# Kernel optimization log

Hardware: AMD Instinct MI355X
Metric: run time of the kernel (lower is better)

Reference implementation:

```python
import jax, jax.numpy as jnp
import numpy as np

NUM_HEADS = 8
ATTN_DIM = 512
DIM_HEAD = ATTN_DIM // NUM_HEADS
SCALE = DIM_HEAD ** -0.5
GN_EPS = 1e-5


def setup_inputs() -> dict:
    key = jax.random.key(0)
    k1, k2, k3 = jax.random.split(key, 3)
    B, H, W, C_IN, C_OUT = 8, 32, 32, 256, 256
    x = jax.random.normal(k1, (B, H, W, C_IN), dtype=jnp.float32)
    w_qkv = jax.random.normal(k2, (C_IN, 3 * ATTN_DIM), dtype=jnp.float32) * (C_IN ** -0.5)
    w_out = jax.random.normal(k3, (ATTN_DIM, C_OUT), dtype=jnp.float32) * (ATTN_DIM ** -0.5)
    b_out = jnp.zeros((C_OUT,), dtype=jnp.float32)
    gamma = jnp.ones((C_OUT,), dtype=jnp.float32)
    beta = jnp.zeros((C_OUT,), dtype=jnp.float32)
    return {"x": x, "w_qkv": w_qkv, "w_out": w_out, "b_out": b_out, "gamma": gamma, "beta": beta}


def reference(x, w_qkv, w_out, b_out, gamma, beta):
    B, H, W, _ = x.shape
    N = H * W
    # 1x1 conv QKV projection (no bias)
    qkv = jnp.einsum('bhwc,cd->bhwd', x, w_qkv)
    q, k, v = jnp.split(qkv, 3, axis=-1)
    # NHWC -> (B, heads, dim_head, HW), matching tf transpose+reshape
    def to_heads(t):
        return t.transpose(0, 3, 1, 2).reshape(B, NUM_HEADS, DIM_HEAD, N)
    q = to_heads(q) * SCALE
    k = to_heads(k)
    v = to_heads(v)
    # sim = q^T k over dim_head: (B, heads, N_q, N_k)
    sim = jnp.einsum('bhcn,bhcm->bhnm', q, k)
    attn = jax.nn.softmax(sim, axis=-1)  # includes the max-subtraction of the original
    # out = attn @ v^T: (B, heads, N, dim_head)
    out = jnp.einsum('bhnm,bhcm->bhnc', attn, v)
    # faithful tf.reshape((B,-1,H,W)) then NCHW->NHWC transpose
    out = out.reshape(B, -1, H, W).transpose(0, 2, 3, 1)  # (B, H, W, attn_dim)
    # output 1x1 conv (with bias) + GroupNorm(groups=1): normalize over (H, W, C) per sample
    y = jnp.einsum('bhwc,cd->bhwd', out, w_out) + b_out
    mean = jnp.mean(y, axis=(1, 2, 3), keepdims=True)
    var = jnp.var(y, axis=(1, 2, 3), keepdims=True)
    y = (y - mean) * jax.lax.rsqrt(var + GN_EPS)
    return y * gamma + beta
```

## Files before the change

### kernel.cpp

```cpp
#include <hip/hip_runtime.h>
#include <math.h>

#define NPOS   1024
#define CIN    256
#define DQKV   1536
#define ATTND  512
#define HEADS  8
#define DH     64
#define COUT   256
#define NBATCH 8
#define SCALE  0.125f
#define GN_EPS 1e-5f

typedef __attribute__((ext_vector_type(8))) __bf16 bf16x8;
typedef __attribute__((ext_vector_type(4))) __bf16 bf16x4;
typedef __attribute__((ext_vector_type(4))) float floatx4;
typedef __attribute__((ext_vector_type(8))) unsigned short ushort8;

#define OFF_XB   (0ull)
#define OFF_WT   (4ull*1048576)
#define OFF_WOT  (4ull*1048576 + 786432ull)
#define OFF_QB   (5ull*1048576)
#define OFF_KB   (13ull*1048576)
#define OFF_VB   (21ull*1048576)
#define OFF_VT   (29ull*1048576)
#define OFF_O2T  (37ull*1048576)
#define OFF_O2TT (45ull*1048576)
#define OFF_ST   (53ull*1048576)

__global__ __launch_bounds__(256) void conv_x(
    const float* __restrict__ x, __bf16* __restrict__ xb, float* __restrict__ stats)
{
    if (blockIdx.x == 0) stats[threadIdx.x] = 0.0f;
    const int i = (blockIdx.x * 256 + threadIdx.x) * 8;
    float4 a = *(const float4*)&x[i];
    float4 b = *(const float4*)&x[i + 4];
    bf16x8 o;
    o[0] = (__bf16)a.x; o[1] = (__bf16)a.y; o[2] = (__bf16)a.z; o[3] = (__bf16)a.w;
    o[4] = (__bf16)b.x; o[5] = (__bf16)b.y; o[6] = (__bf16)b.z; o[7] = (__bf16)b.w;
    *(bf16x8*)&xb[i] = o;
}

__global__ __launch_bounds__(256) void conv_w(
    const float* __restrict__ w, unsigned short* __restrict__ wT)
{
    const int n0 = blockIdx.x * 64, k0 = blockIdx.y * 64;
    __shared__ unsigned short tile[64][68];
    const int t = threadIdx.x;
    #pragma unroll
    for (int p = 0; p < 4; ++p) {
        const int row = p * 16 + (t >> 4);
        const int c = (t & 15) * 4;
        float4 a = *(const float4*)&w[(size_t)(k0 + row) * DQKV + n0 + c];
        float sv[4] = {a.x, a.y, a.z, a.w};
        #pragma unroll
        for (int j = 0; j < 4; ++j) {
            const float sc = (n0 + c + j) < 512 ? SCALE : 1.0f;
            __bf16 hb = (__bf16)(sv[j] * sc);
            tile[row][c + j] = *(unsigned short*)&hb;
        }
    }
    __syncthreads();
    {
        const int nn = t >> 2;
        const int kc = (t & 3) * 16;
        unsigned short tmp[16];
        #pragma unroll
        for (int j = 0; j < 16; ++j) tmp[j] = tile[kc + j][nn];
        *(ushort8*)&wT[(size_t)(n0 + nn) * 256 + k0 + kc]     = *(ushort8*)&tmp[0];
        *(ushort8*)&wT[(size_t)(n0 + nn) * 256 + k0 + kc + 8] = *(ushort8*)&tmp[8];
    }
}

__global__ __launch_bounds__(256) void conv_wo(
    const float* __restrict__ w, unsigned short* __restrict__ woT)
{
    const int d0 = blockIdx.x * 64, k0 = blockIdx.y * 64;
    __shared__ unsigned short tile[64][68];
    const int t = threadIdx.x;
    #pragma unroll
    for (int p = 0; p < 4; ++p) {
        const int row = p * 16 + (t >> 4);
        const int c = (t & 15) * 4;
        float4 a = *(const float4*)&w[(size_t)(k0 + row) * COUT + d0 + c];
        float sv[4] = {a.x, a.y, a.z, a.w};
        #pragma unroll
        for (int j = 0; j < 4; ++j) {
            __bf16 hb = (__bf16)sv[j];
            tile[row][c + j] = *(unsigned short*)&hb;
        }
    }
    __syncthreads();
    {
        const int nn = t >> 2;
        const int kc = (t & 3) * 16;
        unsigned short tmp[16];
        #pragma unroll
        for (int j = 0; j < 16; ++j) tmp[j] = tile[kc + j][nn];
        *(ushort8*)&woT[(size_t)(d0 + nn) * 512 + k0 + kc]     = *(ushort8*)&tmp[0];
        *(ushort8*)&woT[(size_t)(d0 + nn) * 512 + k0 + kc + 8] = *(ushort8*)&tmp[8];
    }
}

__global__ __launch_bounds__(256) void qkv_gemm_mfma(
    const __bf16* __restrict__ xb, const __bf16* __restrict__ wT,
    __bf16* __restrict__ qb, __bf16* __restrict__ kb, __bf16* __restrict__ vb)
{
    const int t = threadIdx.x;
    const int w = t >> 6, lane = t & 63;
    const int col = lane & 15, qd = lane >> 4;
    const int wm = w >> 1, wn = w & 1;
    const int m0 = blockIdx.x * 128, n0 = blockIdx.y * 128;

    __shared__ __align__(16) unsigned short As[128][40];
    __shared__ __align__(16) unsigned short Bs[128][40];

    floatx4 zero4 = {0.f, 0.f, 0.f, 0.f};
    floatx4 acc[4][4];
    #pragma unroll
    for (int i = 0; i < 4; ++i)
        #pragma unroll
        for (int j = 0; j < 4; ++j) acc[i][j] = zero4;

    const int lrow = t >> 2, lc8 = (t & 3) * 8;

    ushort8 areg[2], breg[2];
    areg[0] = *(const ushort8*)&xb[(size_t)(m0 + lrow) * 256 + lc8];
    areg[1] = *(const ushort8*)&xb[(size_t)(m0 + lrow + 64) * 256 + lc8];
    breg[0] = *(const ushort8*)&wT[(size_t)(n0 + lrow) * 256 + lc8];
    breg[1] = *(const ushort8*)&wT[(size_t)(n0 + lrow + 64) * 256 + lc8];

    for (int kk = 0; kk < 8; ++kk) {
        __syncthreads();
        *(ushort8*)&As[lrow][lc8]      = areg[0];
        *(ushort8*)&As[lrow + 64][lc8] = areg[1];
        *(ushort8*)&Bs[lrow][lc8]      = breg[0];
        *(ushort8*)&Bs[lrow + 64][lc8] = breg[1];
        __syncthreads();
        const int kn = (kk < 7) ? (kk + 1) * 32 : 0;
        areg[0] = *(const ushort8*)&xb[(size_t)(m0 + lrow) * 256 + kn + lc8];
        areg[1] = *(const ushort8*)&xb[(size_t)(m0 + lrow + 64) * 256 + kn + lc8];
        breg[0] = *(const ushort8*)&wT[(size_t)(n0 + lrow) * 256 + kn + lc8];
        breg[1] = *(const ushort8*)&wT[(size_t)(n0 + lrow + 64) * 256 + kn + lc8];

        bf16x8 wf[4];
        #pragma unroll
        for (int ct = 0; ct < 4; ++ct)
            wf[ct] = *(const bf16x8*)&Bs[wn * 64 + ct * 16 + col][qd * 8];
        #pragma unroll
        for (int st = 0; st < 4; ++st) {
            bf16x8 xf = *(const bf16x8*)&As[wm * 64 + st * 16 + col][qd * 8];
            #pragma unroll
            for (int ct = 0; ct < 4; ++ct)
                acc[ct][st] = __builtin_amdgcn_mfma_f32_16x16x32_bf16(wf[ct], xf, acc[ct][st], 0, 0, 0);
        }
    }

    #pragma unroll
    for (int ct = 0; ct < 4; ++ct) {
        const int cbase = n0 + wn * 64 + ct * 16;
        const int sect = cbase >> 9;
        const int hh = (cbase >> 6) & 7;
        const int dd = (cbase & 63) + qd * 4;
        __bf16* base = (sect == 0) ? qb : ((sect == 1) ? kb : vb);
        #pragma unroll
        for (int st = 0; st < 4; ++st) {
            const int m = m0 + wm * 64 + st * 16 + col;
            const int b_ = m >> 10, n = m & 1023;
            bf16x4 o;
            #pragma unroll
            for (int r = 0; r < 4; ++r) o[r] = (__bf16)acc[ct][st][r];
            *(bf16x4*)&base[(((size_t)b_ * HEADS + hh) * NPOS + n) * DH + dd] = o;
        }
    }
}

__global__ __launch_bounds__(256) void vtrans(
    const unsigned short* __restrict__ v, unsigned short* __restrict__ vT)
{
    const int bid = blockIdx.x;
    const int bh = bid >> 4, n0 = (bid & 15) * 64;
    __shared__ __align__(16) unsigned short tile[64][72];
    const int t = threadIdx.x;
    #pragma unroll
    for (int p = 0; p < 2; ++p) {
        const int idx = p * 256 + t;
        const int row = idx >> 3, c8 = (idx & 7) * 8;
        *(ushort8*)&tile[row][c8] = *(const ushort8*)&v[((size_t)bh * NPOS + n0 + row) * DH + c8];
    }
    __syncthreads();
    #pragma unroll
    for (int p = 0; p < 2; ++p) {
        const int idx = p * 256 + t;
        const int c = idx >> 3, r8 = (idx & 7) * 8;
        unsigned short tmp[8];
        #pragma unroll
        for (int j = 0; j < 8; ++j) tmp[j] = tile[r8 + j][c];
        *(ushort8*)&vT[((size_t)bh * DH + c) * NPOS + n0 + r8] = *(ushort8*)&tmp[0];
    }
}

__global__ __launch_bounds__(256, 4) void attn_mfma(
    const __bf16* __restrict__ qg, const __bf16* __restrict__ kg,
    const __bf16* __restrict__ vTg, __bf16* __restrict__ o2t)
{
    const int bid = blockIdx.x;
    const int qblk = bid & 15, h = (bid >> 4) & 7, b = bid >> 7;
    const int bh = b * HEADS + h;
    const int t = threadIdx.x;
    const int w = t >> 6, lane = t & 63;
    const int col = lane & 15;
    const int qd = lane >> 4;

    __shared__ __align__(16) unsigned short Ks[64][72];
    __shared__ __align__(16) unsigned short Vts[64][72];
    __shared__ __align__(16) unsigned short ps[4][16][68];

    const __bf16* qptr = qg + ((size_t)bh * NPOS + qblk * 64 + w * 16 + col) * DH;
    const bf16x8 qf0 = *(const bf16x8*)(qptr + qd * 8);
    const bf16x8 qf1 = *(const bf16x8*)(qptr + 32 + qd * 8);

    const unsigned short* kbase  = (const unsigned short*)kg  + (size_t)bh * NPOS * DH;
    const unsigned short* vtbase = (const unsigned short*)vTg + (size_t)bh * DH * NPOS;

    const int r0 = t >> 3, c8 = (t & 7) * 8;

    ushort8 kreg[2], vreg[2];
    kreg[0] = *(const ushort8*)&kbase[(size_t)r0 * DH + c8];
    kreg[1] = *(const ushort8*)&kbase[(size_t)(r0 + 32) * DH + c8];
    vreg[0] = *(const ushort8*)&vtbase[(size_t)r0 * NPOS + c8];
    vreg[1] = *(const ushort8*)&vtbase[(size_t)(r0 + 32) * NPOS + c8];

    floatx4 zero4 = {0.f, 0.f, 0.f, 0.f};
    floatx4 accO[4];
    #pragma unroll
    for (int i = 0; i < 4; ++i) accO[i] = zero4;
    float lsum_acc = 0.0f;

    for (int kt = 0; kt < 16; ++kt) {
        __syncthreads();
        *(ushort8*)&Ks[r0][c8]       = kreg[0];
        *(ushort8*)&Ks[r0 + 32][c8]  = kreg[1];
        *(ushort8*)&Vts[r0][c8]      = vreg[0];
        *(ushort8*)&Vts[r0 + 32][c8] = vreg[1];
        __syncthreads();

        const int ktn = (kt < 15) ? kt + 1 : 15;
        kreg[0] = *(const ushort8*)&kbase[(size_t)(ktn * 64 + r0) * DH + c8];
        kreg[1] = *(const ushort8*)&kbase[(size_t)(ktn * 64 + r0 + 32) * DH + c8];
        vreg[0] = *(const ushort8*)&vtbase[(size_t)r0 * NPOS + ktn * 64 + c8];
        vreg[1] = *(const ushort8*)&vtbase[(size_t)(r0 + 32) * NPOS + ktn * 64 + c8];

        floatx4 accS[4];
        #pragma unroll
        for (int mt = 0; mt < 4; ++mt) accS[mt] = zero4;
        #pragma unroll
        for (int mt = 0; mt < 4; ++mt) {
            bf16x8 kf0 = *(const bf16x8*)&Ks[mt * 16 + col][qd * 8];
            bf16x8 kf1 = *(const bf16x8*)&Ks[mt * 16 + col][32 + qd * 8];
            accS[mt] = __builtin_amdgcn_mfma_f32_16x16x32_bf16(kf0, qf0, accS[mt], 0, 0, 0);
            accS[mt] = __builtin_amdgcn_mfma_f32_16x16x32_bf16(kf1, qf1, accS[mt], 0, 0, 0);
        }

        #pragma unroll
        for (int mt = 0; mt < 4; ++mt) {
            bf16x4 pv;
            #pragma unroll
            for (int r = 0; r < 4; ++r) {
                const float e = __expf(accS[mt][r]);
                lsum_acc += e;
                pv[r] = (__bf16)e;
            }
            *(bf16x4*)&ps[w][col][mt * 16 + qd * 4] = pv;
        }

        const bf16x8 pf0 = *(const bf16x8*)&ps[w][col][qd * 8];
        const bf16x8 pf1 = *(const bf16x8*)&ps[w][col][32 + qd * 8];
        #pragma unroll
        for (int ct = 0; ct < 4; ++ct) {
            bf16x8 vf0 = *(const bf16x8*)&Vts[ct * 16 + col][qd * 8];
            bf16x8 vf1 = *(const bf16x8*)&Vts[ct * 16 + col][32 + qd * 8];
            accO[ct] = __builtin_amdgcn_mfma_f32_16x16x32_bf16(vf0, pf0, accO[ct], 0, 0, 0);
            accO[ct] = __builtin_amdgcn_mfma_f32_16x16x32_bf16(vf1, pf1, accO[ct], 0, 0, 0);
        }
    }

    lsum_acc += __shfl_xor(lsum_acc, 16);
    lsum_acc += __shfl_xor(lsum_acc, 32);
    const float inv_l = 1.0f / lsum_acc;

    const int nrow = qblk * 4 + w;
    const int ch = h * 64 + nrow;
    __bf16* dst = o2t + ((size_t)b * 512 + ch) * NPOS + col * 64;
    #pragma unroll
    for (int ct = 0; ct < 4; ++ct) {
        bf16x4 o;
        #pragma unroll
        for (int r = 0; r < 4; ++r) o[r] = (__bf16)(accO[ct][r] * inv_l);
        *(bf16x4*)&dst[ct * 16 + qd * 4] = o;
    }
}

__global__ __launch_bounds__(256) void ot_trans(
    const unsigned short* __restrict__ o2t, unsigned short* __restrict__ o2tT)
{
    const int bid = blockIdx.x;
    const int b = bid >> 7, cht = (bid >> 4) & 7, pt = bid & 15;
    __shared__ __align__(16) unsigned short tile[64][72];
    const int t = threadIdx.x;
    const unsigned short* src = o2t + ((size_t)b * 512 + cht * 64) * NPOS + pt * 64;
    #pragma unroll
    for (int p = 0; p < 2; ++p) {
        const int idx = p * 256 + t;
        const int row = idx >> 3, c8 = (idx & 7) * 8;
        *(ushort8*)&tile[row][c8] = *(const ushort8*)&src[(size_t)row * NPOS + c8];
    }
    __syncthreads();
    unsigned short* dstb = o2tT + ((size_t)b * NPOS + pt * 64) * ATTND + cht * 64;
    #pragma unroll
    for (int p = 0; p < 2; ++p) {
        const int idx = p * 256 + t;
        const int c = idx >> 3, r8 = (idx & 7) * 8;
        unsigned short tmp[8];
        #pragma unroll
        for (int j = 0; j < 8; ++j) tmp[j] = tile[r8 + j][c];
        *(ushort8*)&dstb[(size_t)c * ATTND + r8] = *(ushort8*)&tmp[0];
    }
}

__global__ __launch_bounds__(256) void out_mfma(
    const __bf16* __restrict__ a, const __bf16* __restrict__ woT,
    const float* __restrict__ b_out, float* __restrict__ y,
    float* __restrict__ stats)
{
    const int t = threadIdx.x;
    const int w = t >> 6, lane = t & 63;
    const int col = lane & 15, qd = lane >> 4;
    const int wm = w >> 1, wn = w & 1;
    const int m0 = blockIdx.x * 64, d0 = blockIdx.y * 64;
    const int b = blockIdx.x >> 4;

    __shared__ __align__(16) unsigned short As[64][72];
    __shared__ __align__(16) unsigned short Bs[64][72];
    __shared__ float reds[4], redq[4];

    floatx4 zero4 = {0.f, 0.f, 0.f, 0.f};
    floatx4 acc[2][2];
    #pragma unroll
    for (int i = 0; i < 2; ++i)
        #pragma unroll
        for (int j = 0; j < 2; ++j) acc[i][j] = zero4;

    const int lrow = t >> 2, lc = (t & 3) * 16;

    for (int k0 = 0; k0 < ATTND; k0 += 64) {
        __syncthreads();
        *(ushort8*)&As[lrow][lc]     = *(const ushort8*)&a[(size_t)(m0 + lrow) * ATTND + k0 + lc];
        *(ushort8*)&As[lrow][lc + 8] = *(const ushort8*)&a[(size_t)(m0 + lrow) * ATTND + k0 + lc + 8];
        *(ushort8*)&Bs[lrow][lc]     = *(const ushort8*)&woT[(size_t)(d0 + lrow) * ATTND + k0 + lc];
        *(ushort8*)&Bs[lrow][lc + 8] = *(const ushort8*)&woT[(size_t)(d0 + lrow) * ATTND + k0 + lc + 8];
        __syncthreads();
        bf16x8 af0[2], af1[2];
        #pragma unroll
        for (int mt = 0; mt < 2; ++mt) {
            af0[mt] = *(const bf16x8*)&As[wm * 32 + mt * 16 + col][qd * 8];
            af1[mt] = *(const bf16x8*)&As[wm * 32 + mt * 16 + col][32 + qd * 8];
        }
        #pragma unroll
        for (int nt = 0; nt < 2; ++nt) {
            bf16x8 bf0 = *(const bf16x8*)&Bs[wn * 32 + nt * 16 + col][qd * 8];
            bf16x8 bf1 = *(const bf16x8*)&Bs[wn * 32 + nt * 16 + col][32 + qd * 8];
            #pragma unroll
            for (int mt = 0; mt < 2; ++mt) {
                acc[mt][nt] = __builtin_amdgcn_mfma_f32_16x16x32_bf16(af0[mt], bf0, acc[mt][nt], 0, 0, 0);
                acc[mt][nt] = __builtin_amdgcn_mfma_f32_16x16x32_bf16(af1[mt], bf1, acc[mt][nt], 0, 0, 0);
            }
        }
    }

    float bias_n[2];
    #pragma unroll
    for (int nt = 0; nt < 2; ++nt) bias_n[nt] = b_out[d0 + wn * 32 + nt * 16 + col];

    float bsum = 0.0f, bsq = 0.0f;
    #pragma unroll
    for (int mt = 0; mt < 2; ++mt) {
        #pragma unroll
        for (int r = 0; r < 4; ++r) {
            const int m = m0 + wm * 32 + mt * 16 + qd * 4 + r;
            const int p = m & 1023;
            #pragma unroll
            for (int nt = 0; nt < 2; ++nt) {
                const int d = d0 + wn * 32 + nt * 16 + col;
                const float v = acc[mt][nt][r] + bias_n[nt];
                y[((size_t)b * NPOS + p) * COUT + d] = v;
                bsum += v;
                bsq  += v * v;
            }
        }
    }
    #pragma unroll
    for (int off = 1; off < 64; off <<= 1) {
        bsum += __shfl_xor(bsum, off);
        bsq  += __shfl_xor(bsq, off);
    }
    if (lane == 0) { reds[w] = bsum; redq[w] = bsq; }
    __syncthreads();
    if (t == 0) {
        atomicAdd(&stats[b * 16],       reds[0] + reds[1] + reds[2] + reds[3]);
        atomicAdd(&stats[128 + b * 16], redq[0] + redq[1] + redq[2] + redq[3]);
    }
}

__global__ __launch_bounds__(256) void gn_finalize(
    float* __restrict__ y, const float* __restrict__ stats,
    const float* __restrict__ gamma, const float* __restrict__ beta)
{
    const int idx = blockIdx.x * 256 + threadIdx.x;
    const int e = idx * 4;
    const int b_ = e >> 18;
    const int d = e & (COUT - 1);
    const float invn = 1.0f / (float)(NPOS * COUT);
    const float mean = stats[b_ * 16] * invn;
    const float var  = stats[128 + b_ * 16] * invn - mean * mean;
    const float rsig = rsqrtf(var + GN_EPS);
    float4 vv = *(float4*)&y[e];
    const float4 g  = *(const float4*)&gamma[d];
    const float4 bt = *(const float4*)&beta[d];
    vv.x = (vv.x - mean) * rsig * g.x + bt.x;
    vv.y = (vv.y - mean) * rsig * g.y + bt.y;
    vv.z = (vv.z - mean) * rsig * g.z + bt.z;
    vv.w = (vv.w - mean) * rsig * g.w + bt.w;
    *(float4*)&y[e] = vv;
}

extern "C" void kernel_launch(void* const* d_in, const int* in_sizes, int n_in,
                              void* d_out, int out_size, void* d_ws, size_t ws_size,
                              hipStream_t stream)
{
    const float* x     = (const float*)d_in[0];
    const float* w_qkv = (const float*)d_in[1];
    const float* w_out = (const float*)d_in[2];
    const float* b_out = (const float*)d_in[3];
    const float* gamma = (const float*)d_in[4];
    const float* beta  = (const float*)d_in[5];
    float* out = (float*)d_out;
    char* ws = (char*)d_ws;

    __bf16* xb  = (__bf16*)(ws + OFF_XB);
    unsigned short* wT  = (unsigned short*)(ws + OFF_WT);
    unsigned short* woT = (unsigned short*)(ws + OFF_WOT);
    __bf16* qb  = (__bf16*)(ws + OFF_QB);
    __bf16* kb  = (__bf16*)(ws + OFF_KB);
    __bf16* vb  = (__bf16*)(ws + OFF_VB);
    unsigned short* vT  = (unsigned short*)(ws + OFF_VT);
    __bf16* o2t  = (__bf16*)(ws + OFF_O2T);
    __bf16* o2tT = (__bf16*)(ws + OFF_O2TT);
    float* stats = (float*)(ws + OFF_ST);

    conv_x       <<<dim3(1024),   256, 0, stream>>>(x, xb, stats);
    conv_w       <<<dim3(24, 4),  256, 0, stream>>>(w_qkv, wT);
    conv_wo      <<<dim3(4, 8),   256, 0, stream>>>(w_out, woT);
    qkv_gemm_mfma<<<dim3(64, 12), 256, 0, stream>>>(xb, (const __bf16*)wT, qb, kb, vb);
    vtrans       <<<dim3(1024),   256, 0, stream>>>((const unsigned short*)vb, vT);
    attn_mfma    <<<dim3(1024),   256, 0, stream>>>(qb, kb, (const __bf16*)vT, o2t);
    ot_trans     <<<dim3(1024),   256, 0, stream>>>((const unsigned short*)o2t, (unsigned short*)o2tT);
    out_mfma     <<<dim3(128, 4), 256, 0, stream>>>(o2tT, (const __bf16*)woT, b_out, out, stats);
    gn_finalize  <<<dim3(2048),   256, 0, stream>>>(out, stats, gamma, beta);
}
```

Baseline: 145.8 us.

## Merge prep kernels and fuse output transpose into attention epilogue

Combines the three input/weight conversion kernels into one launch with block-index dispatch. Removes the separate ot_trans kernel by staging each attention block's output in shared memory (reusing the P buffer) and writing directly in the transposed layout expected by the output GEMM. This drops two launches and a full intermediate read/write of the attention output. The cost is narrower 8-byte scattered global stores in the attention epilogue and an extra block barrier.

```diff
diff --git a/kernel.cpp b/kernel.cpp
--- a/kernel.cpp
+++ b/kernel.cpp
@@ -24,65 +24,65 @@
 #define OFF_KB   (13ull*1048576)
 #define OFF_VB   (21ull*1048576)
 #define OFF_VT   (29ull*1048576)
-#define OFF_O2T  (37ull*1048576)
 #define OFF_O2TT (45ull*1048576)
 #define OFF_ST   (53ull*1048576)
 
-__global__ __launch_bounds__(256) void conv_x(
-    const float* __restrict__ x, __bf16* __restrict__ xb, float* __restrict__ stats)
-{
-    if (blockIdx.x == 0) stats[threadIdx.x] = 0.0f;
-    const int i = (blockIdx.x * 256 + threadIdx.x) * 8;
-    float4 a = *(const float4*)&x[i];
-    float4 b = *(const float4*)&x[i + 4];
-    bf16x8 o;
-    o[0] = (__bf16)a.x; o[1] = (__bf16)a.y; o[2] = (__bf16)a.z; o[3] = (__bf16)a.w;
-    o[4] = (__bf16)b.x; o[5] = (__bf16)b.y; o[6] = (__bf16)b.z; o[7] = (__bf16)b.w;
-    *(bf16x8*)&xb[i] = o;
-}
-
-__global__ __launch_bounds__(256) void conv_w(
-    const float* __restrict__ w, unsigned short* __restrict__ wT)
-{
-    const int n0 = blockIdx.x * 64, k0 = blockIdx.y * 64;
+__global__ __launch_bounds__(256) void prep(
+    const float* __restrict__ x, const float* __restrict__ w_qkv,
+    const float* __restrict__ w_out,
+    __bf16* __restrict__ xb, unsigned short* __restrict__ wT,
+    unsigned short* __restrict__ woT, float* __restrict__ stats)
+{
+    const int bid = blockIdx.x;
+    const int t = threadIdx.x;
     __shared__ unsigned short tile[64][68];
-    const int t = threadIdx.x;
+
+    if (bid < 1024) {
+        if (bid == 0) stats[t] = 0.0f;
+        const int i = (bid * 256 + t) * 8;
+        float4 a = *(const float4*)&x[i];
+        float4 b = *(const float4*)&x[i + 4];
+        bf16x8 o;
+        o[0] = (__bf16)a.x; o[1] = (__bf16)a.y; o[2] = (__bf16)a.z; o[3] = (__bf16)a.w;
+        o[4] = (__bf16)b.x; o[5] = (__bf16)b.y; o[6] = (__bf16)b.z; o[7] = (__bf16)b.w;
+        *(bf16x8*)&xb[i] = o;
+        return;
+    }
+
+    if (bid < 1120) {
+        const int idx = bid - 1024;
+        const int n0 = (idx >> 2) * 64, k0 = (idx & 3) * 64;
+        #pragma unroll
+        for (int p = 0; p < 4; ++p) {
+            const int row = p * 16 + (t >> 4);
+            const int c = (t & 15) * 4;
+            float4 a = *(const float4*)&w_qkv[(size_t)(k0 + row) * DQKV + n0 + c];
+            float sv[4] = {a.x, a.y, a.z, a.w};
+            #pragma unroll
+            for (int j = 0; j < 4; ++j) {
+                const float sc = (n0 + c + j) < 512 ? SCALE : 1.0f;
+                __bf16 hb = (__bf16)(sv[j] * sc);
+                tile[row][c + j] = *(unsigned short*)&hb;
+            }
+        }
+        __syncthreads();
+        const int nn = t >> 2;
+        const int kc = (t & 3) * 16;
+        unsigned short tmp[16];
+        #pragma unroll
+        for (int j = 0; j < 16; ++j) tmp[j] = tile[kc + j][nn];
+        *(ushort8*)&wT[(size_t)(n0 + nn) * 256 + k0 + kc]     = *(ushort8*)&tmp[0];
+        *(ushort8*)&wT[(size_t)(n0 + nn) * 256 + k0 + kc + 8] = *(ushort8*)&tmp[8];
+        return;
+    }
+
+    const int idx = bid - 1120;
+    const int d0 = (idx & 3) * 64, k0 = (idx >> 2) * 64;
     #pragma unroll
     for (int p = 0; p < 4; ++p) {
         const int row = p * 16 + (t >> 4);
         const int c = (t & 15) * 4;
-        float4 a = *(const float4*)&w[(size_t)(k0 + row) * DQKV + n0 + c];
-        float sv[4] = {a.x, a.y, a.z, a.w};
-        #pragma unroll
-        for (int j = 0; j < 4; ++j) {
-            const float sc = (n0 + c + j) < 512 ? SCALE : 1.0f;
-            __bf16 hb = (__bf16)(sv[j] * sc);
-            tile[row][c + j] = *(unsigned short*)&hb;
-        }
-    }
-    __syncthreads();
-    {
-        const int nn = t >> 2;
-        const int kc = (t & 3) * 16;
-        unsigned short tmp[16];
-        #pragma unroll
-        for (int j = 0; j < 16; ++j) tmp[j] = tile[kc + j][nn];
-        *(ushort8*)&wT[(size_t)(n0 + nn) * 256 + k0 + kc]     = *(ushort8*)&tmp[0];
-        *(ushort8*)&wT[(size_t)(n0 + nn) * 256 + k0 + kc + 8] = *(ushort8*)&tmp[8];
-    }
-}
-
-__global__ __launch_bounds__(256) void conv_wo(
-    const float* __restrict__ w, unsigned short* __restrict__ woT)
-{
-    const int d0 = blockIdx.x * 64, k0 = blockIdx.y * 64;
-    __shared__ unsigned short tile[64][68];
-    const int t = threadIdx.x;
-    #pragma unroll
-    for (int p = 0; p < 4; ++p) {
-        const int row = p * 16 + (t >> 4);
-        const int c = (t & 15) * 4;
-        float4 a = *(const float4*)&w[(size_t)(k0 + row) * COUT + d0 + c];
+        float4 a = *(const float4*)&w_out[(size_t)(k0 + row) * COUT + d0 + c];
         float sv[4] = {a.x, a.y, a.z, a.w};
         #pragma unroll
         for (int j = 0; j < 4; ++j) {
@@ -202,7 +202,7 @@
 
 __global__ __launch_bounds__(256, 4) void attn_mfma(
     const __bf16* __restrict__ qg, const __bf16* __restrict__ kg,
-    const __bf16* __restrict__ vTg, __bf16* __restrict__ o2t)
+    const __bf16* __restrict__ vTg, __bf16* __restrict__ o2tT)
 {
     const int bid = blockIdx.x;
     const int qblk = bid & 15, h = (bid >> 4) & 7, b = bid >> 7;
@@ -289,42 +289,28 @@
     lsum_acc += __shfl_xor(lsum_acc, 32);
     const float inv_l = 1.0f / lsum_acc;
 
-    const int nrow = qblk * 4 + w;
-    const int ch = h * 64 + nrow;
-    __bf16* dst = o2t + ((size_t)b * 512 + ch) * NPOS + col * 64;
+    unsigned short (*obuf)[4][68] = (unsigned short (*)[4][68])ps;
+    __syncthreads();
     #pragma unroll
     for (int ct = 0; ct < 4; ++ct) {
         bf16x4 o;
         #pragma unroll
         for (int r = 0; r < 4; ++r) o[r] = (__bf16)(accO[ct][r] * inv_l);
-        *(bf16x4*)&dst[ct * 16 + qd * 4] = o;
-    }
-}
-
-__global__ __launch_bounds__(256) void ot_trans(
-    const unsigned short* __restrict__ o2t, unsigned short* __restrict__ o2tT)
-{
-    const int bid = blockIdx.x;
-    const int b = bid >> 7, cht = (bid >> 4) & 7, pt = bid & 15;
-    __shared__ __align__(16) unsigned short tile[64][72];
-    const int t = threadIdx.x;
-    const unsigned short* src = o2t + ((size_t)b * 512 + cht * 64) * NPOS + pt * 64;
-    #pragma unroll
-    for (int p = 0; p < 2; ++p) {
-        const int idx = p * 256 + t;
-        const int row = idx >> 3, c8 = (idx & 7) * 8;
-        *(ushort8*)&tile[row][c8] = *(const ushort8*)&src[(size_t)row * NPOS + c8];
+        *(bf16x4*)&obuf[col][w][ct * 16 + qd * 4] = o;
     }
     __syncthreads();
-    unsigned short* dstb = o2tT + ((size_t)b * NPOS + pt * 64) * ATTND + cht * 64;
-    #pragma unroll
-    for (int p = 0; p < 2; ++p) {
-        const int idx = p * 256 + t;
-        const int c = idx >> 3, r8 = (idx & 7) * 8;
-        unsigned short tmp[8];
-        #pragma unroll
-        for (int j = 0; j < 8; ++j) tmp[j] = tile[r8 + j][c];
-        *(ushort8*)&dstb[(size_t)c * ATTND + r8] = *(ushort8*)&tmp[0];
+    const int chbase = h * 64 + qblk * 4;
+    #pragma unroll
+    for (int i = 0; i < 4; ++i) {
+        const int p = i * 256 + t;
+        const int pc = p >> 6, cc = p & 63;
+        bf16x4 o;
+        #pragma unroll
+        for (int w4 = 0; w4 < 4; ++w4) {
+            unsigned short u = obuf[pc][w4][cc];
+            o[w4] = *(__bf16*)&u;
+        }
+        *(bf16x4*)&o2tT[((size_t)b * NPOS + p) * ATTND + chbase] = o;
     }
 }
 
@@ -454,17 +440,13 @@
     __bf16* kb  = (__bf16*)(ws + OFF_KB);
     __bf16* vb  = (__bf16*)(ws + OFF_VB);
     unsigned short* vT  = (unsigned short*)(ws + OFF_VT);
-    __bf16* o2t  = (__bf16*)(ws + OFF_O2T);
     __bf16* o2tT = (__bf16*)(ws + OFF_O2TT);
     float* stats = (float*)(ws + OFF_ST);
 
-    conv_x       <<<dim3(1024),   256, 0, stream>>>(x, xb, stats);
-    conv_w       <<<dim3(24, 4),  256, 0, stream>>>(w_qkv, wT);
-    conv_wo      <<<dim3(4, 8),   256, 0, stream>>>(w_out, woT);
+    prep         <<<dim3(1152),   256, 0, stream>>>(x, w_qkv, w_out, xb, wT, woT, stats);
     qkv_gemm_mfma<<<dim3(64, 12), 256, 0, stream>>>(xb, (const __bf16*)wT, qb, kb, vb);
     vtrans       <<<dim3(1024),   256, 0, stream>>>((const unsigned short*)vb, vT);
-    attn_mfma    <<<dim3(1024),   256, 0, stream>>>(qb, kb, (const __bf16*)vT, o2t);
-    ot_trans     <<<dim3(1024),   256, 0, stream>>>((const unsigned short*)o2t, (unsigned short*)o2tT);
+    attn_mfma    <<<dim3(1024),   256, 0, stream>>>(qb, kb, (const __bf16*)vT, o2tT);
     out_mfma     <<<dim3(128, 4), 256, 0, stream>>>(o2tT, (const __bf16*)woT, b_out, out, stats);
     gn_finalize  <<<dim3(2048),   256, 0, stream>>>(out, stats, gamma, beta);
 }
```

New measurement: 142.3 us. 1.02x faster.
